# Kernel tuning notes

Hardware: AMD Instinct MI355X
Metric: run time of the kernel (lower is better)

The kernel has to match this reference:

```python
import jax, jax.numpy as jnp
import numpy as np

B, N, DIM, HEAD = 32, 1024, 512, 8
W_SP = 32  # sqrt(N), query spatial side
SCALE = DIM ** (-0.5)  # original uses full dim, not head_dim
EPS = 1e-5


def setup_inputs() -> dict:
    key = jax.random.key(0)
    ks = jax.random.split(key, 7)
    feats = jax.random.normal(ks[0], (B, N, DIM), dtype=jnp.float32)
    W_q = jax.random.normal(ks[1], (DIM, DIM), dtype=jnp.float32) * (DIM ** -0.5)
    conv_w = jax.random.normal(ks[2], (2 * DIM, DIM, 3, 3), dtype=jnp.float32) * ((DIM * 9) ** -0.5)
    conv_b = jnp.zeros((2 * DIM,), dtype=jnp.float32)
    ln_gamma = jnp.ones((2 * DIM,), dtype=jnp.float32)
    ln_beta = jnp.zeros((2 * DIM,), dtype=jnp.float32)
    W_out = jax.random.normal(ks[3], (DIM, DIM), dtype=jnp.float32) * (DIM ** -0.5)
    return {"feats": feats, "W_q": W_q, "conv_w": conv_w, "conv_b": conv_b,
            "ln_gamma": ln_gamma, "ln_beta": ln_beta, "W_out": W_out}


def reference(feats, W_q, conv_w, conv_b, ln_gamma, ln_beta, W_out):
    b, n, dim = feats.shape
    h = HEAD
    d = dim // h
    # trans_kv: 'b (w h) c -> b c w h' -> conv2d(dim->2dim, k3 s2 p1) -> 'b c w h -> b (w h) c' -> LN
    x = feats.reshape(b, W_SP, W_SP, dim).transpose(0, 3, 1, 2)  # NCHW
    kv = jax.lax.conv_general_dilated(
        x, conv_w, window_strides=(2, 2), padding=((1, 1), (1, 1)),
        dimension_numbers=("NCHW", "OIHW", "NCHW"))
    kv = kv + conv_b[None, :, None, None]          # [b, 2dim, w2, w2]
    m = kv.shape[2] * kv.shape[3]
    kv = kv.reshape(b, 2 * dim, m).transpose(0, 2, 1)  # [b, m, 2dim]
    mu = jnp.mean(kv, axis=-1, keepdims=True)
    var = jnp.var(kv, axis=-1, keepdims=True)
    kv = (kv - mu) * jax.lax.rsqrt(var + EPS) * ln_gamma + ln_beta
    k, v = jnp.split(kv, 2, axis=-1)               # each [b, m, dim]
    q = feats @ W_q.T                               # [b, n, dim]
    q = q.reshape(b, n, h, d)
    k = k.reshape(b, m, h, d)
    v = v.reshape(b, m, h, d)
    alpha = jnp.einsum("bihd,bjhd->bhij", q, k) * SCALE  # [b, h, n, m]
    # NOTE: original computes Conv(alpha) into att, then overwrites with softmax(alpha);
    # the Conv block is dead code w.r.t. the output.
    att = jax.nn.softmax(alpha, axis=-1)
    out = jnp.einsum("bhij,bjhd->bhid", att, v)    # [b, h, n, d]
    out = out.transpose(0, 2, 1, 3).reshape(b, n, dim)
    out = out @ W_out.T                             # fc_out linear (dropout=identity in eval)
    return out
```

## Files before the change

kernel.cpp:

```cpp
#include <hip/hip_runtime.h>
#include <hip/hip_bf16.h>
#include <math.h>

#define B_    32
#define N_    1024
#define DIM_  512
#define HEAD_ 8
#define HD_   64
#define WSP   32
#define M2    256
#define CDIM  1024
#define KCONV 4608
#define KHALF 2304
#define EPS_  1e-5f
#define SCALE_ 0.044194173824159216f
#define PW    34

typedef __attribute__((ext_vector_type(8))) short bf16x8;
typedef __attribute__((ext_vector_type(4))) float f32x4_t;
typedef const __attribute__((address_space(1))) void gas_t;
typedef __attribute__((address_space(3))) void las_t;

__device__ __forceinline__ ushort f2b(float x) {
  __hip_bfloat16 h = __float2bfloat16(x);
  return *reinterpret_cast<const ushort*>(&h);
}

__global__ __launch_bounds__(256) void prep_kernel(
    const float* __restrict__ feats, ushort* __restrict__ featsp,
    const float* __restrict__ W_q, ushort* __restrict__ wqb,
    const float* __restrict__ W_out, ushort* __restrict__ woutb,
    const float* __restrict__ conv_w, ushort* __restrict__ convwb) {
  int blk = blockIdx.x;
  if (blk < 1056) {
    int t = blk * 256 + threadIdx.x;
    int b = t / 8448, r = t - b * 8448;
    int cell = r >> 6, ic8 = (r & 63) * 8;
    int iw, ih;
    if (cell < 34)      { iw = 0;  ih = cell; }
    else if (cell < 68) { iw = 33; ih = cell - 34; }
    else { int e = cell - 68; iw = 1 + (e >> 1); ih = (e & 1) * 33; }
    bf16x8 z = {};
    *reinterpret_cast<bf16x8*>(&featsp[(((size_t)b * PW + iw) * PW + ih) * 512 + ic8]) = z;
  } else if (blk < 1312) {
    int i = (blk - 1056) * 256 + threadIdx.x;
    float4 v = reinterpret_cast<const float4*>(W_q)[i];
    ushort4 o;
    o.x = f2b(v.x); o.y = f2b(v.y); o.z = f2b(v.z); o.w = f2b(v.w);
    reinterpret_cast<ushort4*>(wqb)[i] = o;
  } else if (blk < 1568) {
    int i = (blk - 1312) * 256 + threadIdx.x;
    float4 v = reinterpret_cast<const float4*>(W_out)[i];
    ushort4 o;
    o.x = f2b(v.x); o.y = f2b(v.y); o.z = f2b(v.z); o.w = f2b(v.w);
    reinterpret_cast<ushort4*>(woutb)[i] = o;
  } else if (blk < 20000) {
    int t2 = blk - 1568;
    int oc = t2 / 18, sub = t2 - oc * 18;
    int idx = sub * 256 + threadIdx.x;
    int tap = idx >> 9, ic = idx & 511;
    convwb[(size_t)oc * KCONV + idx] = f2b(conv_w[(size_t)oc * KCONV + ic * 9 + tap]);
  } else {
    int i = (blk - 20000) * 256 + threadIdx.x;
    int e = i * 4;
    int b = e >> 19, r = e & 524287;
    int n = r >> 9, ic = r & 511;
    int iw = n >> 5, ih = n & 31;
    float4 v = reinterpret_cast<const float4*>(feats)[i];
    ushort4 o;
    o.x = f2b(v.x); o.y = f2b(v.y); o.z = f2b(v.z); o.w = f2b(v.w);
    size_t dst = (((size_t)b * PW + iw + 1) * PW + ih + 1) * 512 + ic;
    *reinterpret_cast<ushort4*>(&featsp[dst]) = o;
  }
}

__global__ __launch_bounds__(512, 2) void conv256_kernel(
    const ushort* __restrict__ featsp, const ushort* __restrict__ convwb,
    const float* __restrict__ conv_b, float* __restrict__ kvf,
    float* __restrict__ kvp1) {
  __shared__ __align__(16) ushort lds[2][32768];
  const int tid = threadIdx.x;
  const int lane = tid & 63, wid = tid >> 6;
  const int wr = wid >> 2, wc = wid & 3;
  const int lrow = lane & 15, lk = lane >> 4;
  const int kz = blockIdx.z;
  const int koff = kz * KHALF;

  const int l = blockIdx.y * gridDim.x + blockIdx.x;
  const int v = (l & 7) * 16 + (l >> 3);
  const int bm = (v >> 2) * 256;
  const int bn = (v & 3) * 256;
  const int bimg = bm >> 8;

  f32x4_t acc[8][4] = {};

  auto stage = [&](int buf, int kt) {
    int k0 = koff + (kt << 6);
#pragma unroll
    for (int i = 0; i < 4; ++i) {
      int s = i * 512 + tid;
      int row = s >> 3, ch = s & 7;
      int cl = ch ^ (row & 7);
      int kk = k0 + cl * 8;
      int tap = kk >> 9, ic = kk & 511;
      int kh = tap / 3, kw = tap - 3 * kh;
      int w2 = row >> 4, h2 = row & 15;
      const ushort* ga = &featsp[(((size_t)bimg * PW + 2 * w2 + kh) * PW + 2 * h2 + kw) * 512 + ic];
      __builtin_amdgcn_global_load_lds((gas_t*)ga,
          (las_t*)(&lds[buf][0] + (size_t)s * 8), 16, 0, 0);
    }
#pragma unroll
    for (int i = 0; i < 4; ++i) {
      int s = i * 512 + tid;
      int row = s >> 3, ch = s & 7;
      int cl = ch ^ (row & 7);
      const ushort* gb = &convwb[(size_t)(bn + row) * KCONV + k0 + cl * 8];
      __builtin_amdgcn_global_load_lds((gas_t*)gb,
          (las_t*)(&lds[buf][16384] + (size_t)s * 8), 16, 0, 0);
    }
  };

  const int NT = KHALF >> 6;
  stage(0, 0);
  for (int kt = 0; kt < NT; ++kt) {
    int cur = kt & 1;
    if (kt + 1 < NT) {
      stage(cur ^ 1, kt + 1);
      asm volatile("s_waitcnt vmcnt(8)" ::: "memory");
    } else {
      asm volatile("s_waitcnt vmcnt(0)" ::: "memory");
    }
    __builtin_amdgcn_s_barrier();
    __builtin_amdgcn_sched_barrier(0);
#pragma unroll
    for (int kk = 0; kk < 2; ++kk) {
      bf16x8 aF[8], bF[4];
#pragma unroll
      for (int m = 0; m < 8; ++m) {
        int row = wr * 128 + m * 16 + lrow;
        int ch = (kk * 4 + lk) ^ (row & 7);
        aF[m] = *reinterpret_cast<const bf16x8*>(&lds[cur][row * 64 + ch * 8]);
      }
#pragma unroll
      for (int n = 0; n < 4; ++n) {
        int row = wc * 64 + n * 16 + lrow;
        int ch = (kk * 4 + lk) ^ (row & 7);
        bF[n] = *reinterpret_cast<const bf16x8*>(&lds[cur][16384 + row * 64 + ch * 8]);
      }
#pragma unroll
      for (int m = 0; m < 8; ++m)
#pragma unroll
        for (int n = 0; n < 4; ++n)
          acc[m][n] = __builtin_amdgcn_mfma_f32_16x16x32_bf16(
              aF[m], bF[n], acc[m][n], 0, 0, 0);
    }
    __builtin_amdgcn_sched_barrier(0);
    __builtin_amdgcn_s_barrier();
  }

  float* Co = kz ? kvp1 : kvf;
#pragma unroll
  for (int m = 0; m < 8; ++m) {
#pragma unroll
    for (int n = 0; n < 4; ++n) {
      int col = bn + wc * 64 + n * 16 + lrow;
#pragma unroll
      for (int r = 0; r < 4; ++r) {
        int row = bm + wr * 128 + m * 16 + lk * 4 + r;
        float v2 = acc[m][n][r];
        if (kz == 0) v2 += conv_b[col];
        Co[(size_t)row * CDIM + col] = v2;
      }
    }
  }
}

template<int MODE>
__device__ __forceinline__ void gemm_body(
    ushort (*As)[128][32], ushort (*Bs)[128][32],
    int l, int nbn, int nwg,
    const ushort* __restrict__ A, const ushort* __restrict__ featsp,
    const ushort* __restrict__ Bw, float* __restrict__ Cf,
    ushort* __restrict__ Cb, int M, int N, int K) {
  const int tid = threadIdx.x;
  const int lane = tid & 63, wid = tid >> 6;
  const int wr = wid >> 1, wc = wid & 1;
  const int v = (l & 7) * (nwg >> 3) + (l >> 3);
  const int bm = (v / nbn) * 128, bn = (v % nbn) * 128;
  const int lrow = lane & 15, lk = lane >> 4;
  const int swz = (lrow >> 1) & 3;

  f32x4_t acc[4][4] = {};

  auto stage = [&](int buf, int kt) {
    int k0 = kt << 5;
#pragma unroll
    for (int it = 0; it < 2; ++it) {
      int idx = it * 256 + tid;
      int row = idx >> 2;
      int c = (((idx & 3) ^ ((idx >> 3) & 3))) * 8;
      const ushort* ga;
      if (MODE == 0) {
        ga = &A[(size_t)(bm + row) * K + k0 + c];
      } else {
        int p = bm + row;
        int b = p >> 10, n = p & 1023;
        int iw = n >> 5, ih = n & 31;
        ga = &featsp[(((size_t)b * PW + iw + 1) * PW + ih + 1) * 512 + k0 + c];
      }
      __builtin_amdgcn_global_load_lds((gas_t*)ga,
          (las_t*)(&As[buf][0][0] + (size_t)idx * 8), 16, 0, 0);
      const ushort* gb = &Bw[(size_t)(bn + row) * K + k0 + c];
      __builtin_amdgcn_global_load_lds((gas_t*)gb,
          (las_t*)(&Bs[buf][0][0] + (size_t)idx * 8), 16, 0, 0);
    }
  };

  stage(0, 0);
  const int NT = K >> 5;
  for (int kt = 0; kt < NT; ++kt) {
    int cur = kt & 1;
    if (kt + 1 < NT) {
      stage(cur ^ 1, kt + 1);
      asm volatile("s_waitcnt vmcnt(4)" ::: "memory");
    } else {
      asm volatile("s_waitcnt vmcnt(0)" ::: "memory");
    }
    __builtin_amdgcn_s_barrier();
    __builtin_amdgcn_sched_barrier(0);
    bf16x8 aF[4], bF[4];
#pragma unroll
    for (int m = 0; m < 4; ++m)
      aF[m] = *reinterpret_cast<const bf16x8*>(
          &As[cur][wr * 64 + m * 16 + lrow][(lk ^ swz) * 8]);
#pragma unroll
    for (int n = 0; n < 4; ++n)
      bF[n] = *reinterpret_cast<const bf16x8*>(
          &Bs[cur][wc * 64 + n * 16 + lrow][(lk ^ swz) * 8]);
#pragma unroll
    for (int m = 0; m < 4; ++m)
#pragma unroll
      for (int n = 0; n < 4; ++n)
        acc[m][n] = __builtin_amdgcn_mfma_f32_16x16x32_bf16(
            aF[m], bF[n], acc[m][n], 0, 0, 0);
    __builtin_amdgcn_sched_barrier(0);
    __builtin_amdgcn_s_barrier();
  }

#pragma unroll
  for (int m = 0; m < 4; ++m) {
#pragma unroll
    for (int n = 0; n < 4; ++n) {
      int col = bn + wc * 64 + n * 16 + lrow;
#pragma unroll
      for (int r = 0; r < 4; ++r) {
        int row = bm + wr * 64 + m * 16 + lk * 4 + r;
        float v2 = acc[m][n][r];
        if (MODE == 1) Cb[(size_t)row * N + col] = f2b(v2);
        else Cf[(size_t)row * N + col] = v2;
      }
    }
  }
}

__global__ __launch_bounds__(256) void qproj_kernel(
    const ushort* __restrict__ featsp, const ushort* __restrict__ wqb,
    ushort* __restrict__ qb) {
  __shared__ ushort As[2][128][32];
  __shared__ ushort Bs[2][128][32];
  int l = blockIdx.y * gridDim.x + blockIdx.x;
  gemm_body<1>(As, Bs, l, gridDim.x, gridDim.x * gridDim.y,
               nullptr, featsp, wqb, nullptr, qb, B_ * N_, DIM_, DIM_);
}

__global__ __launch_bounds__(256) void gemm0_kernel(
    const ushort* __restrict__ A, const ushort* __restrict__ Bw,
    float* __restrict__ Cf, int M, int N, int K) {
  __shared__ ushort As[2][128][32];
  __shared__ ushort Bs[2][128][32];
  int l = blockIdx.y * gridDim.x + blockIdx.x;
  gemm_body<0>(As, Bs, l, gridDim.x, gridDim.x * gridDim.y,
               A, nullptr, Bw, Cf, nullptr, M, N, K);
}

__global__ __launch_bounds__(256) void ln_kernel(
    const float* __restrict__ kvp0, const float* __restrict__ kvp1,
    const float* __restrict__ gamma, const float* __restrict__ beta,
    ushort* __restrict__ Kb, ushort* __restrict__ Vb) {
  const int p = blockIdx.x, tid = threadIdx.x;
  float4 a = reinterpret_cast<const float4*>(kvp0 + (size_t)p * CDIM)[tid];
  float4 b4 = reinterpret_cast<const float4*>(kvp1 + (size_t)p * CDIM)[tid];
  float4 x = make_float4(a.x + b4.x, a.y + b4.y, a.z + b4.z, a.w + b4.w);
  float s = x.x + x.y + x.z + x.w;
  float ss = x.x * x.x + x.y * x.y + x.z * x.z + x.w * x.w;
#pragma unroll
  for (int off = 32; off > 0; off >>= 1) {
    s += __shfl_down(s, off);
    ss += __shfl_down(ss, off);
  }
  __shared__ float sb[4], ssb[4];
  if ((tid & 63) == 0) { sb[tid >> 6] = s; ssb[tid >> 6] = ss; }
  __syncthreads();
  float tot = sb[0] + sb[1] + sb[2] + sb[3];
  float tot2 = ssb[0] + ssb[1] + ssb[2] + ssb[3];
  float mu = tot * (1.f / CDIM);
  float var = tot2 * (1.f / CDIM) - mu * mu;
  float rstd = rsqrtf(var + EPS_);
  float4 g = reinterpret_cast<const float4*>(gamma)[tid];
  float4 bb = reinterpret_cast<const float4*>(beta)[tid];
  ushort4 o;
  o.x = f2b((x.x - mu) * rstd * g.x + bb.x);
  o.y = f2b((x.y - mu) * rstd * g.y + bb.y);
  o.z = f2b((x.z - mu) * rstd * g.z + bb.z);
  o.w = f2b((x.w - mu) * rstd * g.w + bb.w);
  int b = p >> 8, j = p & 255;
  int c = tid * 4;
  if (c < DIM_) {
    int h = c >> 6, d = c & 63;
    *reinterpret_cast<ushort4*>(&Kb[(((size_t)(b * 8 + h)) * M2 + j) * HD_ + d]) = o;
  } else {
    int c2 = c - DIM_;
    int h = c2 >> 6, d = c2 & 63;
    *reinterpret_cast<ushort4*>(&Vb[(((size_t)(b * 8 + h)) * M2 + j) * HD_ + d]) = o;
  }
}

__global__ __launch_bounds__(256) void vtrans_kernel(
    const ushort* __restrict__ Vb, ushort* __restrict__ Vt) {
  __shared__ ushort t[64][65];
  const int bh = blockIdx.x, tid = threadIdx.x;
  const ushort* src = Vb + (size_t)bh * M2 * HD_;
  ushort* dst = Vt + (size_t)bh * HD_ * M2;
  for (int j0 = 0; j0 < M2; j0 += 64) {
    __syncthreads();
#pragma unroll
    for (int it = 0; it < 2; ++it) {
      int s = it * 256 + tid;
      int j = s >> 3, d0 = (s & 7) * 8;
      bf16x8 v = *reinterpret_cast<const bf16x8*>(src + (size_t)(j0 + j) * HD_ + d0);
#pragma unroll
      for (int e = 0; e < 8; ++e) t[d0 + e][j] = (ushort)v[e];
    }
    __syncthreads();
#pragma unroll
    for (int it = 0; it < 2; ++it) {
      int s = it * 256 + tid;
      int d = s >> 3, jj0 = (s & 7) * 8;
      bf16x8 o;
#pragma unroll
      for (int e = 0; e < 8; ++e) o[e] = (short)t[d][jj0 + e];
      *reinterpret_cast<bf16x8*>(dst + (size_t)d * M2 + j0 + jj0) = o;
    }
  }
}

__global__ __launch_bounds__(512, 2) void attn_mfma_kernel(
    const ushort* __restrict__ qb, const ushort* __restrict__ Kb,
    const ushort* __restrict__ Vt, ushort* __restrict__ attob) {
  __shared__ __align__(16) char lds[131072];
  char* lp = lds;
  const int tid = threadIdx.x;
  const int lane = tid & 63, wid = tid >> 6;
  const int lr = lane & 15, lk = lane >> 4;
  const int bh = blockIdx.x;
  const int b = bh >> 3, h = bh & 7;

  auto ks_byte = [](int j, int d) -> int {
    return (j << 7) + (((d << 1)) ^ ((j & 7) << 4));
  };
  auto vt_byte = [](int d, int j) -> int {
    return 32768 + (d << 9) + (((j << 1)) ^ ((d & 7) << 4));
  };
  auto p_byte = [](int w, int q4, int kv) -> int {
    return 65536 + (w << 13) + (q4 << 9) + (((kv << 1)) ^ ((q4 & 7) << 4));
  };

  const ushort* Khead  = Kb + (size_t)bh * M2 * HD_;
  const ushort* Vthead = Vt + (size_t)bh * HD_ * M2;

#pragma unroll
  for (int it = 0; it < 4; ++it) {
    int o = (it * 512 + tid) * 16;
    int j = o >> 7, c = (o >> 4) & 7;
    int cl = c ^ (j & 7);
    __builtin_amdgcn_global_load_lds((gas_t*)(Khead + j * HD_ + cl * 8),
        (las_t*)(lp + o), 16, 0, 0);
  }
#pragma unroll
  for (int it = 0; it < 4; ++it) {
    int o = (it * 512 + tid) * 16;
    int d = o >> 9, c = (o >> 4) & 31;
    int cl = c ^ (d & 7);
    __builtin_amdgcn_global_load_lds((gas_t*)(Vthead + d * M2 + cl * 8),
        (las_t*)(lp + 32768 + o), 16, 0, 0);
  }

  __syncthreads();

  for (int qp = 0; qp < 4; ++qp) {
    const int qbase = qp * 256 + wid * 32;
    bf16x8 qf[2][2];
#pragma unroll
    for (int mf = 0; mf < 2; ++mf)
#pragma unroll
      for (int ks = 0; ks < 2; ++ks)
        qf[mf][ks] = *reinterpret_cast<const bf16x8*>(
            qb + ((size_t)(b * N_ + qbase + mf * 16 + lr)) * DIM_ + h * HD_ + ks * 32 + lk * 8);

    f32x4_t sacc[2][16] = {};
    __builtin_amdgcn_s_setprio(1);
#pragma unroll
    for (int ks = 0; ks < 2; ++ks) {
#pragma unroll
      for (int nj = 0; nj < 16; ++nj) {
        bf16x8 kf = *reinterpret_cast<const bf16x8*>(
            lp + ks_byte(nj * 16 + lr, ks * 32 + lk * 8));
        sacc[0][nj] = __builtin_amdgcn_mfma_f32_16x16x32_bf16(qf[0][ks], kf, sacc[0][nj], 0, 0, 0);
        sacc[1][nj] = __builtin_amdgcn_mfma_f32_16x16x32_bf16(qf[1][ks], kf, sacc[1][nj], 0, 0, 0);
      }
    }
    __builtin_amdgcn_s_setprio(0);

    float linv[2][4];
    f32x4_t oacc[2][4] = {};
#pragma unroll
    for (int mf = 0; mf < 2; ++mf) {
#pragma unroll
      for (int r = 0; r < 4; ++r) {
        float pv[16];
        float sum = 0.f;
#pragma unroll
        for (int nj = 0; nj < 16; ++nj) {
          pv[nj] = __expf(sacc[mf][nj][r] * SCALE_);
          sum += pv[nj];
        }
        sum += __shfl_xor(sum, 1);
        sum += __shfl_xor(sum, 2);
        sum += __shfl_xor(sum, 4);
        sum += __shfl_xor(sum, 8);
        linv[mf][r] = 1.f / sum;
        int q4 = lk * 4 + r;
#pragma unroll
        for (int nj = 0; nj < 16; ++nj)
          *reinterpret_cast<ushort*>(lp + p_byte(wid, q4, nj * 16 + lr)) = f2b(pv[nj]);
      }
      __builtin_amdgcn_s_setprio(1);
#pragma unroll
      for (int ks2 = 0; ks2 < 8; ++ks2) {
        bf16x8 pf = *reinterpret_cast<const bf16x8*>(
            lp + p_byte(wid, lr, ks2 * 32 + lk * 8));
#pragma unroll
        for (int df = 0; df < 4; ++df) {
          bf16x8 vf = *reinterpret_cast<const bf16x8*>(
              lp + vt_byte(df * 16 + lr, ks2 * 32 + lk * 8));
          oacc[mf][df] = __builtin_amdgcn_mfma_f32_16x16x32_bf16(pf, vf, oacc[mf][df], 0, 0, 0);
        }
      }
      __builtin_amdgcn_s_setprio(0);
    }

#pragma unroll
    for (int mf = 0; mf < 2; ++mf)
#pragma unroll
      for (int df = 0; df < 4; ++df)
#pragma unroll
        for (int r = 0; r < 4; ++r) {
          int qrow = qbase + mf * 16 + lk * 4 + r;
          int dcol = df * 16 + lr;
          float val = oacc[mf][df][r] * linv[mf][r];
          attob[((size_t)(b * N_ + qrow)) * DIM_ + h * HD_ + dcol] = f2b(val);
        }
  }
}

extern "C" void kernel_launch(void* const* d_in, const int* in_sizes, int n_in,
                              void* d_out, int out_size, void* d_ws, size_t ws_size,
                              hipStream_t stream) {
  const float* feats  = (const float*)d_in[0];
  const float* W_q    = (const float*)d_in[1];
  const float* conv_w = (const float*)d_in[2];
  const float* conv_b = (const float*)d_in[3];
  const float* ln_g   = (const float*)d_in[4];
  const float* ln_b   = (const float*)d_in[5];
  const float* W_out  = (const float*)d_in[6];
  float* out = (float*)d_out;

  const size_t FP_ELEMS = (size_t)B_ * PW * PW * DIM_;
  char* ws = (char*)d_ws;
  ushort* featsp = (ushort*)ws;  ws += FP_ELEMS * 2;
  ushort* qb     = (ushort*)ws;  ws += (size_t)B_ * N_ * DIM_ * 2;
  ushort* attob  = (ushort*)ws;  ws += (size_t)B_ * N_ * DIM_ * 2;
  float*  kvf    = (float*)ws;   ws += (size_t)B_ * M2 * CDIM * 4;
  ushort* convwb = (ushort*)ws;  ws += (size_t)CDIM * KCONV * 2;
  ushort* wqb    = (ushort*)ws;  ws += (size_t)DIM_ * DIM_ * 2;
  ushort* woutb  = (ushort*)ws;  ws += (size_t)DIM_ * DIM_ * 2;
  ushort* Kb     = (ushort*)ws;  ws += (size_t)B_ * HEAD_ * M2 * HD_ * 2;
  ushort* Vt     = (ushort*)ws;  ws += (size_t)B_ * HEAD_ * M2 * HD_ * 2;
  float* kvp1 = (float*)attob;
  ushort* Vb = convwb;

  prep_kernel<<<36384, 256, 0, stream>>>(
      feats, featsp, W_q, wqb, W_out, woutb, conv_w, convwb);

  qproj_kernel<<<dim3(DIM_ / 128, (B_ * N_) / 128), 256, 0, stream>>>(
      featsp, wqb, qb);

  conv256_kernel<<<dim3(CDIM / 256, (B_ * M2) / 256, 2), 512, 0, stream>>>(
      featsp, convwb, conv_b, kvf, kvp1);

  ln_kernel<<<B_ * M2, 256, 0, stream>>>(kvf, kvp1, ln_g, ln_b, Kb, Vb);

  vtrans_kernel<<<B_ * HEAD_, 256, 0, stream>>>(Vb, Vt);

  attn_mfma_kernel<<<B_ * HEAD_, 512, 0, stream>>>(qb, Kb, Vt, attob);

  gemm0_kernel<<<dim3(DIM_ / 128, (B_ * N_) / 128), 256, 0, stream>>>(
      attob, woutb, out, B_ * N_, DIM_, DIM_);
}
```

Measured before the change: 242.7 us.

## Retile Q-projection and output GEMMs to 256x256 tiles with 512 threads

Replaces the 128x128-tile, 256-thread GEMM used for the Q projection and output projection with a 256x256-tile, 512-thread kernel that stages 64-wide K slices and uses an XOR swizzle on 16-byte chunks. Larger tiles raise arithmetic intensity and reduce how often global A/B data is reloaded. The cost is that the grid drops to 256 workgroups, which may underfill the GPU. There is also more LDS (128KB per block) and register pressure from the 8x4 accumulator array.

Result: faster. 232.5 us (median of 2 runs) (-4.2%).

```diff
diff --git a/kernel.cpp b/kernel.cpp
--- a/kernel.cpp
+++ b/kernel.cpp
@@ -176,111 +176,105 @@
 }
 
 template<int MODE>
-__device__ __forceinline__ void gemm_body(
-    ushort (*As)[128][32], ushort (*Bs)[128][32],
-    int l, int nbn, int nwg,
+__global__ __launch_bounds__(512, 2) void gemm256_kernel(
     const ushort* __restrict__ A, const ushort* __restrict__ featsp,
     const ushort* __restrict__ Bw, float* __restrict__ Cf,
-    ushort* __restrict__ Cb, int M, int N, int K) {
+    ushort* __restrict__ Cb) {
+  __shared__ __align__(16) ushort lds[2][32768];
   const int tid = threadIdx.x;
   const int lane = tid & 63, wid = tid >> 6;
-  const int wr = wid >> 1, wc = wid & 1;
-  const int v = (l & 7) * (nwg >> 3) + (l >> 3);
-  const int bm = (v / nbn) * 128, bn = (v % nbn) * 128;
+  const int wr = wid >> 2, wc = wid & 3;
   const int lrow = lane & 15, lk = lane >> 4;
-  const int swz = (lrow >> 1) & 3;
-
-  f32x4_t acc[4][4] = {};
+
+  const int l = blockIdx.y * gridDim.x + blockIdx.x;
+  const int v = (l & 7) * 32 + (l >> 3);
+  const int bm = (v >> 1) * 256;
+  const int bn = (v & 1) * 256;
+
+  f32x4_t acc[8][4] = {};
 
   auto stage = [&](int buf, int kt) {
-    int k0 = kt << 5;
-#pragma unroll
-    for (int it = 0; it < 2; ++it) {
-      int idx = it * 256 + tid;
-      int row = idx >> 2;
-      int c = (((idx & 3) ^ ((idx >> 3) & 3))) * 8;
+    int k0 = kt << 6;
+#pragma unroll
+    for (int i = 0; i < 4; ++i) {
+      int s = i * 512 + tid;
+      int row = s >> 3, ch = s & 7;
+      int cl = ch ^ (row & 7);
       const ushort* ga;
-      if (MODE == 0) {
-        ga = &A[(size_t)(bm + row) * K + k0 + c];
-      } else {
+      if (MODE == 1) {
         int p = bm + row;
         int b = p >> 10, n = p & 1023;
         int iw = n >> 5, ih = n & 31;
-        ga = &featsp[(((size_t)b * PW + iw + 1) * PW + ih + 1) * 512 + k0 + c];
+        ga = &featsp[(((size_t)b * PW + iw + 1) * PW + ih + 1) * 512 + k0 + cl * 8];
+      } else {
+        ga = &A[(size_t)(bm + row) * DIM_ + k0 + cl * 8];
       }
       __builtin_amdgcn_global_load_lds((gas_t*)ga,
-          (las_t*)(&As[buf][0][0] + (size_t)idx * 8), 16, 0, 0);
-      const ushort* gb = &Bw[(size_t)(bn + row) * K + k0 + c];
+          (las_t*)(&lds[buf][0] + (size_t)s * 8), 16, 0, 0);
+    }
+#pragma unroll
+    for (int i = 0; i < 4; ++i) {
+      int s = i * 512 + tid;
+      int row = s >> 3, ch = s & 7;
+      int cl = ch ^ (row & 7);
+      const ushort* gb = &Bw[(size_t)(bn + row) * DIM_ + k0 + cl * 8];
       __builtin_amdgcn_global_load_lds((gas_t*)gb,
-          (las_t*)(&Bs[buf][0][0] + (size_t)idx * 8), 16, 0, 0);
+          (las_t*)(&lds[buf][16384] + (size_t)s * 8), 16, 0, 0);
     }
   };
 
+  const int NT = DIM_ >> 6;
   stage(0, 0);
-  const int NT = K >> 5;
   for (int kt = 0; kt < NT; ++kt) {
     int cur = kt & 1;
     if (kt + 1 < NT) {
       stage(cur ^ 1, kt + 1);
-      asm volatile("s_waitcnt vmcnt(4)" ::: "memory");
+      asm volatile("s_waitcnt vmcnt(8)" ::: "memory");
     } else {
       asm volatile("s_waitcnt vmcnt(0)" ::: "memory");
     }
     __builtin_amdgcn_s_barrier();
     __builtin_amdgcn_sched_barrier(0);
-    bf16x8 aF[4], bF[4];
-#pragma unroll
-    for (int m = 0; m < 4; ++m)
-      aF[m] = *reinterpret_cast<const bf16x8*>(
-          &As[cur][wr * 64 + m * 16 + lrow][(lk ^ swz) * 8]);
-#pragma unroll
-    for (int n = 0; n < 4; ++n)
-      bF[n] = *reinterpret_cast<const bf16x8*>(
-          &Bs[cur][wc * 64 + n * 16 + lrow][(lk ^ swz) * 8]);
-#pragma unroll
-    for (int m = 0; m < 4; ++m)
-#pragma unroll
-      for (int n = 0; n < 4; ++n)
-        acc[m][n] = __builtin_amdgcn_mfma_f32_16x16x32_bf16(
-            aF[m], bF[n], acc[m][n], 0, 0, 0);
+#pragma unroll
+    for (int kk = 0; kk < 2; ++kk) {
+      bf16x8 aF[8], bF[4];
+#pragma unroll
+      for (int m = 0; m < 8; ++m) {
+        int row = wr * 128 + m * 16 + lrow;
+        int ch = (kk * 4 + lk) ^ (row & 7);
+        aF[m] = *reinterpret_cast<const bf16x8*>(&lds[cur][row * 64 + ch * 8]);
+      }
+#pragma unroll
+      for (int n = 0; n < 4; ++n) {
+        int row = wc * 64 + n * 16 + lrow;
+        int ch = (kk * 4 + lk) ^ (row & 7);
+        bF[n] = *reinterpret_cast<const bf16x8*>(&lds[cur][16384 + row * 64 + ch * 8]);
+      }
+#pragma unroll
+      for (int m = 0; m < 8; ++m)
+#pragma unroll
+        for (int n = 0; n < 4; ++n)
+          acc[m][n] = __builtin_amdgcn_mfma_f32_16x16x32_bf16(
+              aF[m], bF[n], acc[m][n], 0, 0, 0);
+    }
     __builtin_amdgcn_sched_barrier(0);
     __builtin_amdgcn_s_barrier();
   }
 
 #pragma unroll
-  for (int m = 0; m < 4; ++m) {
+  for (int m = 0; m < 8; ++m) {
 #pragma unroll
     for (int n = 0; n < 4; ++n) {
       int col = bn + wc * 64 + n * 16 + lrow;
 #pragma unroll
       for (int r = 0; r < 4; ++r) {
-        int row = bm + wr * 64 + m * 16 + lk * 4 + r;
+        int row = bm + wr * 128 + m * 16 + lk * 4 + r;
         float v2 = acc[m][n][r];
-        if (MODE == 1) Cb[(size_t)row * N + col] = f2b(v2);
-        else Cf[(size_t)row * N + col] = v2;
-      }
-    }
-  }
-}
-
-__global__ __launch_bounds__(256) void qproj_kernel(
-    const ushort* __restrict__ featsp, const ushort* __restrict__ wqb,
-    ushort* __restrict__ qb) {
-  __shared__ ushort As[2][128][32];
-  __shared__ ushort Bs[2][128][32];
-  int l = blockIdx.y * gridDim.x + blockIdx.x;
-  gemm_body<1>(As, Bs, l, gridDim.x, gridDim.x * gridDim.y,
-               nullptr, featsp, wqb, nullptr, qb, B_ * N_, DIM_, DIM_);
-}
-
-__global__ __launch_bounds__(256) void gemm0_kernel(
-    const ushort* __restrict__ A, const ushort* __restrict__ Bw,
-    float* __restrict__ Cf, int M, int N, int K) {
-  __shared__ ushort As[2][128][32];
-  __shared__ ushort Bs[2][128][32];
-  int l = blockIdx.y * gridDim.x + blockIdx.x;
-  gemm_body<0>(As, Bs, l, gridDim.x, gridDim.x * gridDim.y,
-               A, nullptr, Bw, Cf, nullptr, M, N, K);
+        if (MODE == 1) Cb[(size_t)row * DIM_ + col] = f2b(v2);
+        else Cf[(size_t)row * DIM_ + col] = v2;
+      }
+    }
+  }
 }
 
 __global__ __launch_bounds__(256) void ln_kernel(
@@ -502,8 +496,8 @@
   prep_kernel<<<36384, 256, 0, stream>>>(
       feats, featsp, W_q, wqb, W_out, woutb, conv_w, convwb);
 
-  qproj_kernel<<<dim3(DIM_ / 128, (B_ * N_) / 128), 256, 0, stream>>>(
-      featsp, wqb, qb);
+  gemm256_kernel<1><<<dim3(2, 128), 512, 0, stream>>>(
+      nullptr, featsp, wqb, nullptr, qb);
 
   conv256_kernel<<<dim3(CDIM / 256, (B_ * M2) / 256, 2), 512, 0, stream>>>(
       featsp, convwb, conv_b, kvf, kvp1);
@@ -514,6 +508,6 @@
 
   attn_mfma_kernel<<<B_ * HEAD_, 512, 0, stream>>>(qb, Kb, Vt, attob);
 
-  gemm0_kernel<<<dim3(DIM_ / 128, (B_ * N_) / 128), 256, 0, stream>>>(
-      attob, woutb, out, B_ * N_, DIM_, DIM_);
-}
+  gemm256_kernel<0><<<dim3(2, 128), 512, 0, stream>>>(
+      attob, nullptr, woutb, out, nullptr);
+}
```
